# Optimization experiments

Measured on AMD Instinct MI355X. Metric: run time of the kernel, lower is better.

Reference implementation:

```python
import jax, jax.numpy as jnp
import numpy as np

N = 16000
E = 512000
HID = 128
OUT = 64
BN_EPS = 1e-5


def setup_inputs() -> dict:
    key = jax.random.key(0)
    ks = jax.random.split(key, 8)
    x = jax.random.normal(ks[0], (N, HID), dtype=jnp.float32)
    src = jax.random.randint(ks[1], (E,), 0, N, dtype=jnp.int32)
    dst = jax.random.randint(ks[2], (E,), 0, N, dtype=jnp.int32)
    s = 1.0 / np.sqrt(HID)
    fc_w = jax.random.uniform(ks[3], (OUT, HID), jnp.float32, -s, s)
    fc_b = jnp.zeros((OUT,), jnp.float32)
    w1 = jax.random.uniform(ks[4], (HID, HID), jnp.float32, -s, s)
    b1 = jnp.zeros((HID,), jnp.float32)
    w2 = jax.random.uniform(ks[5], (OUT, HID), jnp.float32, -s, s)
    b2 = jnp.zeros((OUT,), jnp.float32)
    epsilon = jnp.full((N,), 0.5, jnp.float32)
    gamma = jnp.ones((OUT,), jnp.float32)
    beta = jnp.zeros((OUT,), jnp.float32)
    return {"x": x, "src": src, "dst": dst, "fc_w": fc_w, "fc_b": fc_b,
            "w1": w1, "b1": b1, "w2": w2, "b2": b2,
            "epsilon": epsilon, "gamma": gamma, "beta": beta}


def _agg(feat, src, dst, n):
    # DGL update_all(copy_src, sum): gather source features, scatter-sum to dst.
    return jax.ops.segment_sum(feat[src], dst, num_segments=n)


def reference(x, src, dst, fc_w, fc_b, w1, b1, w2, b2, epsilon, gamma, beta):
    n = x.shape[0]
    # skip-path linear projection
    h1 = x @ fc_w.T + fc_b                       # [N, OUT]
    # GraphConv layer 1: aggregate then linear, then ReLU
    h2 = jax.nn.relu(_agg(x, src, dst, n) @ w1.T + b1)   # [N, HID]
    # GraphConv layer 2
    h2 = _agg(h2, src, dst, n) @ w2.T + b2       # [N, OUT]
    # per-node epsilon blend
    eps = epsilon[:, None]
    h = (1.0 - eps) * h1 + eps * h2              # [N, OUT]
    # averaged gram matrices
    ret = (h @ h.T + x @ x.T) * 0.5              # [N, N]
    # BatchNorm1d (training mode: biased batch stats)
    mean = jnp.mean(h, axis=0)
    var = jnp.mean(jnp.square(h - mean), axis=0)
    hn = (h - mean) * jax.lax.rsqrt(var + BN_EPS) * gamma + beta
    return ret, hn
```

## Files before the change

### kernel.cpp

```cpp
#include <hip/hip_runtime.h>
#include <hip/hip_bf16.h>

typedef __bf16 bf16x8 __attribute__((ext_vector_type(8)));
typedef float  f32x4  __attribute__((ext_vector_type(4)));

#define HID 128
#define OUT 64
#define GK  192
#define BN_EPS 1e-5f

__device__ __forceinline__ float bf2f(unsigned short u) {
  union { unsigned int i; float f; } c; c.i = ((unsigned)u) << 16; return c.f;
}

__global__ __launch_bounds__(256) void hist_k(
    const int* __restrict__ dst, int* __restrict__ cnt, int e)
{
  int stride = gridDim.x * blockDim.x;
  for (int i = blockIdx.x * blockDim.x + threadIdx.x; i < e; i += stride)
    atomicAdd(&cnt[dst[i]], 1);
}

__global__ __launch_bounds__(256) void scan_k(
    const int* __restrict__ cnt, int* __restrict__ offsets,
    int* __restrict__ cursor, int n)
{
  __shared__ int part[256];
  int t = threadIdx.x;
  int chunk = (n + 255) / 256;
  int base = t * chunk;
  int s = 0;
  for (int i = 0; i < chunk; ++i) {
    int idx = base + i;
    if (idx < n) s += cnt[idx];
  }
  part[t] = s;
  __syncthreads();
  for (int off = 1; off < 256; off <<= 1) {
    int v = 0;
    if (t >= off) v = part[t - off];
    __syncthreads();
    if (t >= off) part[t] += v;
    __syncthreads();
  }
  int run = (t == 0) ? 0 : part[t - 1];
  for (int i = 0; i < chunk; ++i) {
    int idx = base + i;
    if (idx < n) {
      offsets[idx] = run;
      cursor[idx]  = run;
      run += cnt[idx];
    }
  }
  if (t == 255) offsets[n] = run;
}

__global__ __launch_bounds__(256) void place_k(
    const int* __restrict__ src, const int* __restrict__ dst,
    int* __restrict__ cursor, int* __restrict__ sorted_src, int e)
{
  int stride = gridDim.x * blockDim.x;
  for (int i = blockIdx.x * blockDim.x + threadIdx.x; i < e; i += stride) {
    int pos = atomicAdd(&cursor[dst[i]], 1);
    sorted_src[pos] = src[i];
  }
}

__global__ __launch_bounds__(256) void agg_k(
    const float* __restrict__ feat, const int* __restrict__ sorted_src,
    const int* __restrict__ offsets, float* __restrict__ agg, int n)
{
  int wave = (blockIdx.x * 256 + threadIdx.x) >> 6;
  int lane = threadIdx.x & 63;
  if (wave >= n) return;
  int half = lane >> 5;
  int l32  = lane & 31;
  int beg = offsets[wave], end = offsets[wave + 1];
  f32x4 a0 = {0.f, 0.f, 0.f, 0.f}, a1 = {0.f, 0.f, 0.f, 0.f};
  int i = beg + half;
  for (; i + 2 < end; i += 4) {
    int s0 = sorted_src[i];
    int s1 = sorted_src[i + 2];
    a0 += *(const f32x4*)(feat + (size_t)s0 * HID + l32 * 4);
    a1 += *(const f32x4*)(feat + (size_t)s1 * HID + l32 * 4);
  }
  if (i < end) {
    int s0 = sorted_src[i];
    a0 += *(const f32x4*)(feat + (size_t)s0 * HID + l32 * 4);
  }
  a0 += a1;
  f32x4 other;
  #pragma unroll
  for (int j = 0; j < 4; ++j) other[j] = __shfl_xor(a0[j], 32, 64);
  a0 += other;
  if (half == 0)
    *(f32x4*)(agg + (size_t)wave * HID + l32 * 4) = a0;
}

__global__ __launch_bounds__(256) void agg2y_k(
    const unsigned short* __restrict__ y2, const int* __restrict__ sorted_src,
    const int* __restrict__ offsets, float* __restrict__ aggy, int n)
{
  int wave = (blockIdx.x * 256 + threadIdx.x) >> 6;
  int lane = threadIdx.x & 63;
  if (wave >= n) return;
  int qtr = lane >> 4;
  int l16 = lane & 15;
  int beg = offsets[wave], end = offsets[wave + 1];
  f32x4 a0 = {0.f, 0.f, 0.f, 0.f}, a1 = {0.f, 0.f, 0.f, 0.f};
  int i = beg + qtr;
  for (; i + 4 < end; i += 8) {
    int s0 = sorted_src[i];
    int s1 = sorted_src[i + 4];
    ushort4 v0 = *(const ushort4*)(y2 + (size_t)s0 * OUT + l16 * 4);
    ushort4 v1 = *(const ushort4*)(y2 + (size_t)s1 * OUT + l16 * 4);
    a0[0] += bf2f(v0.x); a0[1] += bf2f(v0.y); a0[2] += bf2f(v0.z); a0[3] += bf2f(v0.w);
    a1[0] += bf2f(v1.x); a1[1] += bf2f(v1.y); a1[2] += bf2f(v1.z); a1[3] += bf2f(v1.w);
  }
  if (i < end) {
    int s0 = sorted_src[i];
    ushort4 v0 = *(const ushort4*)(y2 + (size_t)s0 * OUT + l16 * 4);
    a0[0] += bf2f(v0.x); a0[1] += bf2f(v0.y); a0[2] += bf2f(v0.z); a0[3] += bf2f(v0.w);
  }
  a0 += a1;
  f32x4 other;
  #pragma unroll
  for (int j = 0; j < 4; ++j) other[j] = __shfl_xor(a0[j], 16, 64);
  a0 += other;
  #pragma unroll
  for (int j = 0; j < 4; ++j) other[j] = __shfl_xor(a0[j], 32, 64);
  a0 += other;
  if (qtr == 0)
    *(f32x4*)(aggy + (size_t)wave * OUT + l16 * 4) = a0;
}

__global__ __launch_bounds__(256) void mlp_fused_k(
    const float* __restrict__ agg, const float* __restrict__ w1,
    const float* __restrict__ b1, const float* __restrict__ w2,
    unsigned short* __restrict__ y2, int n)
{
  __shared__ float aggs[16][132];
  __shared__ float h2s[16][132];
  int t = threadIdx.x;
  int rbase = blockIdx.x * 16;

  for (int idx = t; idx < 16 * 32; idx += 256) {
    int r = idx >> 5, c = idx & 31;
    ((f32x4*)&aggs[r][0])[c] = ((const f32x4*)(agg + (size_t)(rbase + r) * HID))[c];
  }
  __syncthreads();

  {
    int j = t & 127, rh = t >> 7;
    const f32x4* w1r = (const f32x4*)(w1 + (size_t)j * HID);
    float acc[8];
    float bj = b1[j];
    #pragma unroll
    for (int p = 0; p < 8; ++p) acc[p] = bj;
    for (int k = 0; k < 32; ++k) {
      f32x4 w = w1r[k];
      #pragma unroll
      for (int p = 0; p < 8; ++p) {
        f32x4 a = ((const f32x4*)&aggs[rh * 8 + p][0])[k];
        acc[p] += w[0] * a[0] + w[1] * a[1] + w[2] * a[2] + w[3] * a[3];
      }
    }
    #pragma unroll
    for (int p = 0; p < 8; ++p) h2s[rh * 8 + p][j] = fmaxf(acc[p], 0.f);
  }
  __syncthreads();

  {
    int o = t & 63, rq = t >> 6;
    const f32x4* w2r = (const f32x4*)(w2 + (size_t)o * HID);
    float acc[4] = {0.f, 0.f, 0.f, 0.f};
    for (int k = 0; k < 32; ++k) {
      f32x4 w = w2r[k];
      #pragma unroll
      for (int p = 0; p < 4; ++p) {
        f32x4 a = ((const f32x4*)&h2s[rq + p * 4][0])[k];
        acc[p] += w[0] * a[0] + w[1] * a[1] + w[2] * a[2] + w[3] * a[3];
      }
    }
    #pragma unroll
    for (int p = 0; p < 4; ++p) {
      __bf16 b = (__bf16)acc[p];
      y2[(size_t)(rbase + rq + p * 4) * OUT + o] = *(unsigned short*)&b;
    }
  }
}

__global__ __launch_bounds__(256) void combine_k(
    const float* __restrict__ x, const float* __restrict__ aggy,
    const float* __restrict__ fcw, const float* __restrict__ fcb,
    const float* __restrict__ b2,
    const float* __restrict__ eps, float* __restrict__ h,
    __bf16* __restrict__ G, float* __restrict__ stats, int n)
{
  __shared__ float xs[32][132];
  __shared__ float ls[256], lss[256];
  int t = threadIdx.x;
  int rbase = blockIdx.x * 32;

  for (int idx = t; idx < 32 * 32; idx += 256) {
    int r = idx >> 5, c = idx & 31;
    ((f32x4*)&xs[r][0])[c] = ((const f32x4*)(x + (size_t)(rbase + r) * HID))[c];
  }
  __syncthreads();

  int o = t & 63, rq = t >> 6;
  const f32x4* fwr = (const f32x4*)(fcw + (size_t)o * HID);
  float fb = fcb[o], bb = b2[o];
  float acc[8];
  #pragma unroll
  for (int p = 0; p < 8; ++p) acc[p] = fb;
  for (int k = 0; k < 32; ++k) {
    f32x4 w = fwr[k];
    #pragma unroll
    for (int p = 0; p < 8; ++p) {
      f32x4 a = ((const f32x4*)&xs[rq + p * 4][0])[k];
      acc[p] += w[0] * a[0] + w[1] * a[1] + w[2] * a[2] + w[3] * a[3];
    }
  }
  float s = 0.f, ss = 0.f;
  #pragma unroll
  for (int p = 0; p < 8; ++p) {
    int row = rbase + rq + p * 4;
    float a2 = aggy[(size_t)row * OUT + o] + bb;
    float ev = eps[row];
    float hv = (1.f - ev) * acc[p] + ev * a2;
    h[(size_t)row * OUT + o] = hv;
    G[(size_t)row * GK + o] = (__bf16)hv;
    s += hv; ss += hv * hv;
  }
  for (int idx = t; idx < 32 * 64; idx += 256) {
    int rr = idx >> 6, cp = idx & 63;
    int row = rbase + rr;
    float xa = xs[rr][cp * 2], xb = xs[rr][cp * 2 + 1];
    G[(size_t)row * GK + OUT + cp * 2]     = (__bf16)xa;
    G[(size_t)row * GK + OUT + cp * 2 + 1] = (__bf16)xb;
  }
  ls[t] = s; lss[t] = ss;
  __syncthreads();
  if (t < 64) {
    s  = ls[t]  + ls[t + 64]  + ls[t + 128]  + ls[t + 192];
    ss = lss[t] + lss[t + 64] + lss[t + 128] + lss[t + 192];
    atomicAdd(&stats[t], s);
    atomicAdd(&stats[64 + t], ss);
  }
}

__global__ __launch_bounds__(256) void hn_k(
    const float* __restrict__ h, const float* __restrict__ stats,
    const float* __restrict__ gamma, const float* __restrict__ beta,
    float* __restrict__ outp, int n)
{
  int stride = gridDim.x * blockDim.x;
  int total  = n * OUT;
  float inv_n = 1.f / (float)n;
  for (int idx = blockIdx.x * blockDim.x + threadIdx.x; idx < total; idx += stride) {
    int col = idx & 63;
    float mean = stats[col] * inv_n;
    float var  = stats[64 + col] * inv_n - mean * mean;
    float sc   = rsqrtf(var + BN_EPS) * gamma[col];
    outp[idx] = (h[idx] - mean) * sc + beta[col];
  }
}

__global__ __launch_bounds__(256, 3) void gemm_k(
    const __bf16* __restrict__ G, float* __restrict__ out, int n, int nwg)
{
  __shared__ char pool[64 * 132 * 4];
  __bf16* As = (__bf16*)pool;
  __bf16* Bs = (__bf16*)(pool + 16384);
  float*  T  = (float*)pool;

  int nb = n >> 7;
  int orig = blockIdx.x;
  int q = nwg >> 3, r = nwg & 7;
  int xcd = orig & 7, idx8 = orig >> 3;
  int bid = (xcd < r ? xcd * (q + 1) : r * (q + 1) + (xcd - r) * q) + idx8;

  int bi = 0, rem = bid;
  while (rem >= nb - bi) { rem -= nb - bi; ++bi; }
  int bj = bi + rem;
  int t = threadIdx.x;
  int w = t >> 6, lane = t & 63;
  int wr = (w >> 1) << 6;
  int wc = (w & 1) << 6;
  int lr = lane & 15, lg = lane >> 4;

  const uint4* ga = (const uint4*)(G + (size_t)bi * 128 * GK);
  const uint4* gb = (const uint4*)(G + (size_t)bj * 128 * GK);
  uint4* Asv = (uint4*)As;
  uint4* Bsv = (uint4*)Bs;

  f32x4 acc[4][4] = {};
  #pragma unroll
  for (int kc = 0; kc < 3; ++kc) {
    #pragma unroll
    for (int it = 0; it < 4; ++it) {
      int ch = t + it * 256;
      int row = ch >> 3, c = ch & 7;
      int sw = row * 8 + (c ^ (row & 7));
      int gidx = row * 24 + kc * 8 + c;
      Asv[sw] = ga[gidx];
      Bsv[sw] = gb[gidx];
    }
    __syncthreads();
    const bf16x8* Ac = (const bf16x8*)As;
    const bf16x8* Bc = (const bf16x8*)Bs;
    #pragma unroll
    for (int ks = 0; ks < 2; ++ks) {
      bf16x8 a[4], b[4];
      #pragma unroll
      for (int m = 0; m < 4; ++m) {
        int ar = wr + m * 16 + lr;
        int br = wc + m * 16 + lr;
        a[m] = Ac[ar * 8 + ((ks * 4 + lg) ^ (ar & 7))];
        b[m] = Bc[br * 8 + ((ks * 4 + lg) ^ (br & 7))];
      }
      #pragma unroll
      for (int m = 0; m < 4; ++m)
        #pragma unroll
        for (int nn = 0; nn < 4; ++nn)
          acc[m][nn] = __builtin_amdgcn_mfma_f32_16x16x32_bf16(a[m], b[nn], acc[m][nn], 0, 0, 0);
    }
    __syncthreads();
  }

  #pragma unroll
  for (int m = 0; m < 4; ++m)
    #pragma unroll
    for (int nn = 0; nn < 4; ++nn)
      acc[m][nn] = acc[m][nn] * 0.5f;

  size_t N = (size_t)n;

  if (bi != bj) {
    #pragma unroll
    for (int p = 0; p < 2; ++p) {
      if ((wc >> 6) == p) {
        #pragma unroll
        for (int m = 0; m < 4; ++m)
          #pragma unroll
          for (int nn = 0; nn < 4; ++nn) {
            int c  = nn * 16 + lr;
            int r0 = wr + m * 16 + lg * 4;
            *(f32x4*)&T[c * 132 + r0] = acc[m][nn];
          }
      }
      __syncthreads();
      #pragma unroll
      for (int it = 0; it < 8; ++it) {
        int idx = t + it * 256;
        int rr = idx >> 5, c4 = idx & 31;
        f32x4 v = *(const f32x4*)&T[rr * 132 + c4 * 4];
        *(f32x4*)&out[(size_t)(bj * 128 + p * 64 + rr) * N + bi * 128 + c4 * 4] = v;
      }
      __syncthreads();
    }
  }

  #pragma unroll
  for (int m = 0; m < 4; ++m) {
    size_t gr0 = (size_t)(bi * 128 + wr + m * 16 + lg * 4);
    #pragma unroll
    for (int nn = 0; nn < 4; ++nn) {
      int gc = bj * 128 + wc + nn * 16 + lr;
      #pragma unroll
      for (int r = 0; r < 4; ++r)
        out[(gr0 + r) * N + gc] = acc[m][nn][r];
    }
  }
}

extern "C" void kernel_launch(void* const* d_in, const int* in_sizes, int n_in,
                              void* d_out, int out_size, void* d_ws, size_t ws_size,
                              hipStream_t stream) {
  const float* x    = (const float*)d_in[0];
  const int*   src  = (const int*)d_in[1];
  const int*   dst  = (const int*)d_in[2];
  const float* fcw  = (const float*)d_in[3];
  const float* fcb  = (const float*)d_in[4];
  const float* w1   = (const float*)d_in[5];
  const float* b1   = (const float*)d_in[6];
  const float* w2   = (const float*)d_in[7];
  const float* b2   = (const float*)d_in[8];
  const float* eps  = (const float*)d_in[9];
  const float* gamma= (const float*)d_in[10];
  const float* beta = (const float*)d_in[11];
  int n = in_sizes[0] / HID;
  int e = in_sizes[1];
  float* out = (float*)d_out;

  char* ws = (char*)d_ws;
  size_t off = 0;
  float* agg   = (float*)(ws + off); off += (size_t)n * HID * 4;
  float* h     = (float*)(ws + off); off += (size_t)n * OUT * 4;
  __bf16* G    = (__bf16*)(ws + off); off += (size_t)n * GK * 2;
  float* stats = (float*)(ws + off); off += 512;
  unsigned short* y2 = (unsigned short*)(ws + off); off += (size_t)n * OUT * 2;
  float* aggy  = (float*)(ws + off); off += (size_t)n * OUT * 4;
  int* cnt     = (int*)(ws + off); off += (size_t)n * 4;
  int* offsets = (int*)(ws + off); off += (size_t)(n + 1) * 4;
  int* cursor  = (int*)(ws + off); off += (size_t)n * 4;
  int* sorted_src = (int*)(ws + off); off += (size_t)e * 4;

  hipMemsetAsync(cnt, 0, (size_t)n * 4, stream);
  hipMemsetAsync(stats, 0, 2 * OUT * 4, stream);

  hist_k<<<512, 256, 0, stream>>>(dst, cnt, e);
  scan_k<<<1, 256, 0, stream>>>(cnt, offsets, cursor, n);
  place_k<<<512, 256, 0, stream>>>(src, dst, cursor, sorted_src, e);

  agg_k<<<(n * 64 + 255) / 256, 256, 0, stream>>>(x, sorted_src, offsets, agg, n);
  mlp_fused_k<<<n / 16, 256, 0, stream>>>(agg, w1, b1, w2, y2, n);
  agg2y_k<<<(n * 64 + 255) / 256, 256, 0, stream>>>(y2, sorted_src, offsets, aggy, n);
  combine_k<<<n / 32, 256, 0, stream>>>(x, aggy, fcw, fcb, b2, eps, h, G, stats, n);
  hn_k<<<1024, 256, 0, stream>>>(h, stats, gamma, beta, out + (size_t)n * n, n);

  int nb = n >> 7;
  int nwg = nb * (nb + 1) / 2;
  gemm_k<<<nwg, 256, 0, stream>>>(G, out, n, nwg);
}
```

Before: 414.7 us.

## Convert x to bf16 up front and aggregate layer-1 from bf16 features

Adds a kernel that converts x to bf16 once and zeroes the degree counts, replacing the memsets. The first-layer gather now reads bf16 rows (half the bytes per edge) and accumulates in fp32. The concatenated G buffer is split into separate h and x bf16 buffers that the gram GEMM reads directly, so combine_k no longer writes x. This cuts gather bandwidth and a few launches but rounds x to bf16 before aggregation, which loses some accuracy in layer 1.

```diff
diff --git a/kernel.cpp b/kernel.cpp
--- a/kernel.cpp
+++ b/kernel.cpp
@@ -3,14 +3,32 @@
 
 typedef __bf16 bf16x8 __attribute__((ext_vector_type(8)));
 typedef float  f32x4  __attribute__((ext_vector_type(4)));
+typedef unsigned short u16x8 __attribute__((ext_vector_type(8)));
 
 #define HID 128
 #define OUT 64
-#define GK  192
 #define BN_EPS 1e-5f
 
 __device__ __forceinline__ float bf2f(unsigned short u) {
   union { unsigned int i; float f; } c; c.i = ((unsigned)u) << 16; return c.f;
+}
+
+__global__ __launch_bounds__(256) void xconv_k(
+    const float* __restrict__ x, unsigned short* __restrict__ xbf,
+    int* __restrict__ cnt, int n)
+{
+  int gid = blockIdx.x * blockDim.x + threadIdx.x;
+  if (gid < n) cnt[gid] = 0;
+  int stride = gridDim.x * blockDim.x;
+  int total = n * 32;
+  for (int idx = gid; idx < total; idx += stride) {
+    f32x4 v = ((const f32x4*)x)[idx];
+    ushort4 o;
+    __bf16 b0 = (__bf16)v[0], b1 = (__bf16)v[1], b2 = (__bf16)v[2], b3 = (__bf16)v[3];
+    o.x = *(unsigned short*)&b0; o.y = *(unsigned short*)&b1;
+    o.z = *(unsigned short*)&b2; o.w = *(unsigned short*)&b3;
+    ((ushort4*)xbf)[idx] = o;
+  }
 }
 
 __global__ __launch_bounds__(256) void hist_k(
@@ -23,10 +41,11 @@
 
 __global__ __launch_bounds__(256) void scan_k(
     const int* __restrict__ cnt, int* __restrict__ offsets,
-    int* __restrict__ cursor, int n)
-{
+    int* __restrict__ cursor, float* __restrict__ stats, int n)
+{
+  int t = threadIdx.x;
+  if (t < 128) stats[t] = 0.f;
   __shared__ int part[256];
-  int t = threadIdx.x;
   int chunk = (n + 255) / 256;
   int base = t * chunk;
   int s = 0;
@@ -66,35 +85,44 @@
   }
 }
 
-__global__ __launch_bounds__(256) void agg_k(
-    const float* __restrict__ feat, const int* __restrict__ sorted_src,
+__global__ __launch_bounds__(256) void aggx_k(
+    const unsigned short* __restrict__ xbf, const int* __restrict__ sorted_src,
     const int* __restrict__ offsets, float* __restrict__ agg, int n)
 {
   int wave = (blockIdx.x * 256 + threadIdx.x) >> 6;
   int lane = threadIdx.x & 63;
   if (wave >= n) return;
-  int half = lane >> 5;
-  int l32  = lane & 31;
+  int qtr = lane >> 4;
+  int l16 = lane & 15;
   int beg = offsets[wave], end = offsets[wave + 1];
-  f32x4 a0 = {0.f, 0.f, 0.f, 0.f}, a1 = {0.f, 0.f, 0.f, 0.f};
-  int i = beg + half;
-  for (; i + 2 < end; i += 4) {
+  float a0[8] = {}, a1[8] = {};
+  int i = beg + qtr;
+  for (; i + 4 < end; i += 8) {
     int s0 = sorted_src[i];
-    int s1 = sorted_src[i + 2];
-    a0 += *(const f32x4*)(feat + (size_t)s0 * HID + l32 * 4);
-    a1 += *(const f32x4*)(feat + (size_t)s1 * HID + l32 * 4);
+    int s1 = sorted_src[i + 4];
+    u16x8 v0 = *(const u16x8*)(xbf + (size_t)s0 * HID + l16 * 8);
+    u16x8 v1 = *(const u16x8*)(xbf + (size_t)s1 * HID + l16 * 8);
+    #pragma unroll
+    for (int j = 0; j < 8; ++j) { a0[j] += bf2f(v0[j]); a1[j] += bf2f(v1[j]); }
   }
   if (i < end) {
     int s0 = sorted_src[i];
-    a0 += *(const f32x4*)(feat + (size_t)s0 * HID + l32 * 4);
-  }
-  a0 += a1;
-  f32x4 other;
-  #pragma unroll
-  for (int j = 0; j < 4; ++j) other[j] = __shfl_xor(a0[j], 32, 64);
-  a0 += other;
-  if (half == 0)
-    *(f32x4*)(agg + (size_t)wave * HID + l32 * 4) = a0;
+    u16x8 v0 = *(const u16x8*)(xbf + (size_t)s0 * HID + l16 * 8);
+    #pragma unroll
+    for (int j = 0; j < 8; ++j) a0[j] += bf2f(v0[j]);
+  }
+  #pragma unroll
+  for (int j = 0; j < 8; ++j) a0[j] += a1[j];
+  #pragma unroll
+  for (int j = 0; j < 8; ++j) a0[j] += __shfl_xor(a0[j], 16, 64);
+  #pragma unroll
+  for (int j = 0; j < 8; ++j) a0[j] += __shfl_xor(a0[j], 32, 64);
+  if (qtr == 0) {
+    f32x4 lo = {a0[0], a0[1], a0[2], a0[3]};
+    f32x4 hi = {a0[4], a0[5], a0[6], a0[7]};
+    *(f32x4*)(agg + (size_t)wave * HID + l16 * 8)     = lo;
+    *(f32x4*)(agg + (size_t)wave * HID + l16 * 8 + 4) = hi;
+  }
 }
 
 __global__ __launch_bounds__(256) void agg2y_k(
@@ -195,7 +223,7 @@
     const float* __restrict__ fcw, const float* __restrict__ fcb,
     const float* __restrict__ b2,
     const float* __restrict__ eps, float* __restrict__ h,
-    __bf16* __restrict__ G, float* __restrict__ stats, int n)
+    unsigned short* __restrict__ hbf, float* __restrict__ stats, int n)
 {
   __shared__ float xs[32][132];
   __shared__ float ls[256], lss[256];
@@ -230,15 +258,9 @@
     float ev = eps[row];
     float hv = (1.f - ev) * acc[p] + ev * a2;
     h[(size_t)row * OUT + o] = hv;
-    G[(size_t)row * GK + o] = (__bf16)hv;
+    __bf16 hb = (__bf16)hv;
+    hbf[(size_t)row * OUT + o] = *(unsigned short*)&hb;
     s += hv; ss += hv * hv;
-  }
-  for (int idx = t; idx < 32 * 64; idx += 256) {
-    int rr = idx >> 6, cp = idx & 63;
-    int row = rbase + rr;
-    float xa = xs[rr][cp * 2], xb = xs[rr][cp * 2 + 1];
-    G[(size_t)row * GK + OUT + cp * 2]     = (__bf16)xa;
-    G[(size_t)row * GK + OUT + cp * 2 + 1] = (__bf16)xb;
   }
   ls[t] = s; lss[t] = ss;
   __syncthreads();
@@ -268,7 +290,8 @@
 }
 
 __global__ __launch_bounds__(256, 3) void gemm_k(
-    const __bf16* __restrict__ G, float* __restrict__ out, int n, int nwg)
+    const unsigned short* __restrict__ hbf, const unsigned short* __restrict__ xbf,
+    float* __restrict__ out, int n, int nwg)
 {
   __shared__ char pool[64 * 132 * 4];
   __bf16* As = (__bf16*)pool;
@@ -290,8 +313,10 @@
   int wc = (w & 1) << 6;
   int lr = lane & 15, lg = lane >> 4;
 
-  const uint4* ga = (const uint4*)(G + (size_t)bi * 128 * GK);
-  const uint4* gb = (const uint4*)(G + (size_t)bj * 128 * GK);
+  const uint4* ha = (const uint4*)(hbf + (size_t)bi * 128 * OUT);
+  const uint4* hb = (const uint4*)(hbf + (size_t)bj * 128 * OUT);
+  const uint4* xa = (const uint4*)(xbf + (size_t)bi * 128 * HID);
+  const uint4* xb = (const uint4*)(xbf + (size_t)bj * 128 * HID);
   uint4* Asv = (uint4*)As;
   uint4* Bsv = (uint4*)Bs;
 
@@ -303,9 +328,11 @@
       int ch = t + it * 256;
       int row = ch >> 3, c = ch & 7;
       int sw = row * 8 + (c ^ (row & 7));
-      int gidx = row * 24 + kc * 8 + c;
-      Asv[sw] = ga[gidx];
-      Bsv[sw] = gb[gidx];
+      uint4 va, vb;
+      if (kc == 0) { va = ha[row * 8 + c];                  vb = hb[row * 8 + c]; }
+      else         { va = xa[row * 16 + (kc - 1) * 8 + c];  vb = xb[row * 16 + (kc - 1) * 8 + c]; }
+      Asv[sw] = va;
+      Bsv[sw] = vb;
     }
     __syncthreads();
     const bf16x8* Ac = (const bf16x8*)As;
@@ -398,29 +425,28 @@
   size_t off = 0;
   float* agg   = (float*)(ws + off); off += (size_t)n * HID * 4;
   float* h     = (float*)(ws + off); off += (size_t)n * OUT * 4;
-  __bf16* G    = (__bf16*)(ws + off); off += (size_t)n * GK * 2;
+  float* aggy  = (float*)(ws + off); off += (size_t)n * OUT * 4;
+  unsigned short* xbf = (unsigned short*)(ws + off); off += (size_t)n * HID * 2;
+  unsigned short* hbf = (unsigned short*)(ws + off); off += (size_t)n * OUT * 2;
+  unsigned short* y2  = (unsigned short*)(ws + off); off += (size_t)n * OUT * 2;
   float* stats = (float*)(ws + off); off += 512;
-  unsigned short* y2 = (unsigned short*)(ws + off); off += (size_t)n * OUT * 2;
-  float* aggy  = (float*)(ws + off); off += (size_t)n * OUT * 4;
   int* cnt     = (int*)(ws + off); off += (size_t)n * 4;
   int* offsets = (int*)(ws + off); off += (size_t)(n + 1) * 4;
   int* cursor  = (int*)(ws + off); off += (size_t)n * 4;
   int* sorted_src = (int*)(ws + off); off += (size_t)e * 4;
 
-  hipMemsetAsync(cnt, 0, (size_t)n * 4, stream);
-  hipMemsetAsync(stats, 0, 2 * OUT * 4, stream);
-
+  xconv_k<<<2048, 256, 0, stream>>>(x, xbf, cnt, n);
   hist_k<<<512, 256, 0, stream>>>(dst, cnt, e);
-  scan_k<<<1, 256, 0, stream>>>(cnt, offsets, cursor, n);
+  scan_k<<<1, 256, 0, stream>>>(cnt, offsets, cursor, stats, n);
   place_k<<<512, 256, 0, stream>>>(src, dst, cursor, sorted_src, e);
 
-  agg_k<<<(n * 64 + 255) / 256, 256, 0, stream>>>(x, sorted_src, offsets, agg, n);
+  aggx_k<<<(n * 64 + 255) / 256, 256, 0, stream>>>(xbf, sorted_src, offsets, agg, n);
   mlp_fused_k<<<n / 16, 256, 0, stream>>>(agg, w1, b1, w2, y2, n);
   agg2y_k<<<(n * 64 + 255) / 256, 256, 0, stream>>>(y2, sorted_src, offsets, aggy, n);
-  combine_k<<<n / 32, 256, 0, stream>>>(x, aggy, fcw, fcb, b2, eps, h, G, stats, n);
+  combine_k<<<n / 32, 256, 0, stream>>>(x, aggy, fcw, fcb, b2, eps, h, hbf, stats, n);
   hn_k<<<1024, 256, 0, stream>>>(h, stats, gamma, beta, out + (size_t)n * n, n);
 
   int nb = n >> 7;
   int nwg = nb * (nb + 1) / 2;
-  gemm_k<<<nwg, 256, 0, stream>>>(G, out, n, nwg);
-}
+  gemm_k<<<nwg, 256, 0, stream>>>(hbf, xbf, out, n, nwg);
+}
```

After: 398.6 us. 3.9% less time.
